# Kernel tuning notes

Measured on AMD Instinct MI355X. Metric: run time of the kernel, lower is better.

## Reference

```python
import jax, jax.numpy as jnp
import numpy as np

B, S, E, H, L, A, OBS = 4, 1024, 512, 8, 4, 8, 128
D_HEAD = E // H
EPS = 1e-6
DECAY_SCALING = 1.0


def rmsnorm(x, scale):
    return x * jax.lax.rsqrt(jnp.mean(x * x, -1, keepdims=True) + EPS) * scale


def swiglu_ffn(x, w_gate, w_lin, w_out):
    return (jax.nn.silu(x @ w_gate) * (x @ w_lin)) @ w_out


def retention(x, h, logk, w_q, w_k, w_v, w_g, w_o, gns, gnb, ts, seg):
    # x:[B,S,E]  h:[B,H,d,d]  ts/seg:[B,S] int  logk:[H]
    q = (x @ w_q).reshape(B, S, H, D_HEAD).transpose(0, 2, 1, 3)
    k = (x @ w_k).reshape(B, S, H, D_HEAD).transpose(0, 2, 1, 3) / jnp.sqrt(jnp.asarray(D_HEAD, x.dtype))
    v = (x @ w_v).reshape(B, S, H, D_HEAD).transpose(0, 2, 1, 3)
    dt = (ts[:, :, None] - ts[:, None, :]).astype(x.dtype)            # [B,S,S]
    mask = (dt >= 0) & (seg[:, :, None] == seg[:, None, :])           # timestep-causal, same episode
    dt = jnp.where(mask, dt, 0.0)
    Dm = jnp.where(mask[:, None], jnp.exp(dt[:, None] * logk[None, :, None, None]), 0.0)  # [B,H,S,S]
    scores = jnp.einsum('bhnd,bhmd->bhnm', q, k) * Dm
    inner = jnp.einsum('bhnm,bhme->bhne', scores, v)
    tsf = ts.astype(x.dtype)
    fresh = (seg == 0).astype(x.dtype)                                # prev-chunk state only valid pre-done
    xi = jnp.exp((tsf + 1.0)[:, None, :] * logk[None, :, None]) * fresh[:, None, :]  # [B,H,S]
    cross = jnp.einsum('bhn,bhnd,bhde->bhne', xi, q, h)
    ret = inner + cross                                               # [B,H,S,d]
    # chunk-final recurrent state
    tmax = tsf[:, -1]
    eta = jnp.exp((tmax[:, None] - tsf)[:, None, :] * logk[None, :, None])
    eta = eta * (seg == seg[:, -1:]).astype(x.dtype)[:, None, :]
    keep = (seg[:, -1] == 0).astype(x.dtype)
    h_decay = jnp.exp((tmax + 1.0)[:, None] * logk[None, :]) * keep[:, None]  # [B,H]
    h_new = h * h_decay[..., None, None] + jnp.einsum('bhm,bhmd,bhme->bhde', eta, k, v)
    # per-head group norm (num_groups = n_head)
    y = ret.transpose(0, 2, 1, 3)                                     # [B,S,H,d]
    mu = jnp.mean(y, -1, keepdims=True)
    var = jnp.mean((y - mu) ** 2, -1, keepdims=True)
    y = ((y - mu) * jax.lax.rsqrt(var + EPS)).reshape(B, S, E) * gns + gnb
    out = (jax.nn.silu(x @ w_g) * y) @ w_o
    return out, h_new


def forward(obs, hstate, dones, timestep_id, ln_enc_scale, w_enc, ln_shared,
            wq, wk, wv, wg, wo, gn_scale, gn_bias, ln1_s, ln2_s,
            sw_gate, sw_lin, sw_out, head_w1, head_b1, head_ln, head_w2, head_b2):
    kappas = (1.0 - jnp.exp(jnp.linspace(jnp.log(1.0 / 32.0), jnp.log(1.0 / 512.0), H))) * DECAY_SCALING
    logk = jnp.log(kappas).astype(obs.dtype)
    seg = jnp.cumsum(dones, axis=-1)
    x = jax.nn.gelu(rmsnorm(obs, ln_enc_scale) @ w_enc)               # obs encoder
    new_h = jnp.zeros_like(hstate)
    for i in range(L):
        xin = rmsnorm(x, ln_shared)
        ret, hn = retention(xin, hstate[:, :, i], logk, wq[i], wk[i], wv[i], wg[i], wo[i],
                            gn_scale[i], gn_bias[i], timestep_id, seg)
        x1 = rmsnorm(xin + ret, ln1_s[i])
        x = rmsnorm(x1 + swiglu_ffn(x1, sw_gate[i], sw_lin[i], sw_out[i]), ln2_s[i])
        new_h = new_h.at[:, :, i].set(hn)
    z = jax.nn.gelu(x @ head_w1 + head_b1)
    v_loc = rmsnorm(z, head_ln) @ head_w2 + head_b2
    return v_loc, x, new_h


def setup_inputs() -> dict:
    key = jax.random.key(0)
    ks = jax.random.split(key, 16)
    sc = 0.02
    f = jnp.float32
    return {
        'obs': jax.random.normal(ks[0], (B, S, OBS), f),
        'hstate': jax.random.normal(ks[1], (B, H, L, D_HEAD, D_HEAD), f) * 0.1,
        'dones': (jax.random.uniform(ks[2], (B, S)) < 0.01).astype(jnp.int32),
        'timestep_id': jnp.broadcast_to(jnp.repeat(jnp.arange(S // A, dtype=jnp.int32), A)[None], (B, S)),
        'ln_enc_scale': jnp.ones((OBS,), f),
        'w_enc': jax.random.normal(ks[3], (OBS, E), f) * sc,
        'ln_shared': jnp.ones((E,), f),
        'wq': jax.random.normal(ks[4], (L, E, E), f) * sc,
        'wk': jax.random.normal(ks[5], (L, E, E), f) * sc,
        'wv': jax.random.normal(ks[6], (L, E, E), f) * sc,
        'wg': jax.random.normal(ks[7], (L, E, E), f) * sc,
        'wo': jax.random.normal(ks[8], (L, E, E), f) * sc,
        'gn_scale': jnp.ones((L, E), f),
        'gn_bias': jnp.zeros((L, E), f),
        'ln1_s': jnp.ones((L, E), f),
        'ln2_s': jnp.ones((L, E), f),
        'sw_gate': jax.random.normal(ks[9], (L, E, E), f) * sc,
        'sw_lin': jax.random.normal(ks[10], (L, E, E), f) * sc,
        'sw_out': jax.random.normal(ks[11], (L, E, E), f) * sc,
        'head_w1': jax.random.normal(ks[12], (E, E), f) * sc,
        'head_b1': jnp.zeros((E,), f),
        'head_ln': jnp.ones((E,), f),
        'head_w2': jax.random.normal(ks[13], (E, 1), f) * 0.01,
        'head_b2': jnp.zeros((1,), f),
    }


def reference(obs, hstate, dones, timestep_id, ln_enc_scale, w_enc, ln_shared,
              wq, wk, wv, wg, wo, gn_scale, gn_bias, ln1_s, ln2_s,
              sw_gate, sw_lin, sw_out, head_w1, head_b1, head_ln, head_w2, head_b2):
    return forward(obs, hstate, dones, timestep_id, ln_enc_scale, w_enc, ln_shared,
                   wq, wk, wv, wg, wo, gn_scale, gn_bias, ln1_s, ln2_s,
                   sw_gate, sw_lin, sw_out, head_w1, head_b1, head_ln, head_w2, head_b2)
```

## Files before the change

kernel.cpp:

```cpp
#include <hip/hip_runtime.h>
#include <math.h>

#define BN 4
#define SN 1024
#define EN 512
#define HN 8
#define LN 4
#define DN 64
#define OBSN 128
#define NR (BN*SN)
#define NB (NR*EN)
#define EPSF 1e-6f

typedef __attribute__((ext_vector_type(8))) short short8v;
typedef __attribute__((ext_vector_type(4))) float f32x4;
typedef unsigned short u16;

__device__ __forceinline__ float logk_of(int h){
    const float start = -3.4657359027997265f;
    const float step  = -0.3960841031771117f;
    return logf(1.0f - expf(start + step*(float)h));
}
__device__ __forceinline__ float geluf(float x){
    float x3 = x*x*x;
    return 0.5f*x*(1.0f + tanhf(0.7978845608028654f*(x + 0.044715f*x3)));
}
__device__ __forceinline__ float siluf(float x){
    return x / (1.0f + expf(-x));
}
__device__ __forceinline__ u16 f2bf(float x){
    union { float f; unsigned u; } v; v.f = x;
    unsigned r = v.u + 0x7FFFu + ((v.u >> 16) & 1u);
    return (u16)(r >> 16);
}
__device__ __forceinline__ float bf2f(u16 x){
    union { unsigned u; float f; } v; v.u = ((unsigned)x)<<16;
    return v.f;
}
__device__ __forceinline__ void load_lds16(const void* g, void* l){
    __builtin_amdgcn_global_load_lds((const __attribute__((address_space(1))) void*)g,
                                     (__attribute__((address_space(3))) void*)l, 16, 0, 0);
}
__device__ __forceinline__ int swz(int r, int bo){ return r*128 + (bo ^ ((r&7)<<4)); }

__global__ void seg_kernel(const int* __restrict__ dones, int* __restrict__ seg){
    __shared__ int sm[SN];
    int b = blockIdx.x, t = threadIdx.x;
    sm[t] = dones[b*SN + t];
    __syncthreads();
    for (int off=1; off<SN; off<<=1){
        int v = (t>=off) ? sm[t-off] : 0;
        __syncthreads();
        sm[t] += v;
        __syncthreads();
    }
    seg[b*SN + t] = sm[t];
}

__global__ void wconv8_kernel(const float* w0, const float* w1, const float* w2,
                              const float* w3, const float* w4, const float* w5,
                              const float* w6, const float* w7,
                              u16* __restrict__ dst){
    __shared__ u16 tile[32][33];
    int z = blockIdx.z;
    int type = z>>2, layer = z&3;
    const float* srcs[8] = {w0,w1,w2,w3,w4,w5,w6,w7};
    const float* s = srcs[type] + (size_t)layer*EN*EN;
    u16* d = dst + ((size_t)type*LN + layer)*EN*EN;
    int k0 = blockIdx.y*32, m0 = blockIdx.x*32;
    int tx = threadIdx.x, ty = threadIdx.y;
    #pragma unroll
    for (int i=0;i<32;i+=8)
        tile[tx][ty+i] = f2bf(s[(size_t)(k0+ty+i)*EN + m0+tx]);
    __syncthreads();
    #pragma unroll
    for (int i=0;i<32;i+=8)
        d[(size_t)(m0+ty+i)*EN + k0+tx] = tile[ty+i][tx];
}
__global__ void wconv_kernel(const float* __restrict__ src, u16* __restrict__ dst,
                             int K, int M){
    __shared__ u16 tile[32][33];
    int k0 = blockIdx.y*32, m0 = blockIdx.x*32;
    int tx = threadIdx.x, ty = threadIdx.y;
    #pragma unroll
    for (int i=0;i<32;i+=8)
        tile[tx][ty+i] = f2bf(src[(size_t)(k0+ty+i)*M + m0+tx]);
    __syncthreads();
    #pragma unroll
    for (int i=0;i<32;i+=8)
        dst[(size_t)(m0+ty+i)*K + k0+tx] = tile[ty+i][tx];
}

template<int COLS, bool WF32, bool WBF>
__global__ void rmsnorm_kernel(const float* __restrict__ A,
                               const float* __restrict__ scale,
                               float* __restrict__ Of,
                               u16* __restrict__ Ob){
    constexpr int PER = COLS/64;
    int row  = blockIdx.x*4 + (threadIdx.x>>6);
    int lane = threadIdx.x & 63;
    const float* a = A + (size_t)row*COLS;
    float v[PER];
    float ss = 0.f;
    #pragma unroll
    for (int i=0;i<PER;i++){
        float x = a[lane + i*64];
        v[i] = x; ss += x*x;
    }
    #pragma unroll
    for (int off=32; off>0; off>>=1) ss += __shfl_xor(ss, off, 64);
    float rs = rsqrtf(ss*(1.0f/COLS) + EPSF);
    #pragma unroll
    for (int i=0;i<PER;i++){
        float o = v[i]*rs*scale[lane + i*64];
        if (WF32) Of[(size_t)row*COLS + lane + i*64] = o;
        if (WBF)  Ob[(size_t)row*COLS + lane + i*64] = f2bf(o);
    }
}

__device__ __forceinline__ void stage_tile(const u16* __restrict__ G, size_t rowBase,
                                           int K, int k0, u16* dst, int t){
    #pragma unroll
    for (int i=0;i<2;i++){
        int o = i*4096 + t*16;
        int grow = o>>7, gcolb = o&127;
        load_lds16(G + (rowBase+grow)*K + k0 + (gcolb>>1), (char*)dst + o);
    }
}
__device__ __forceinline__ void mma_tile(const u16* As, const u16* Bs, f32x4 acc[2][2],
                                         int wr, int wc, int lane){
    #pragma unroll
    for (int kk=0; kk<64; kk+=32){
        int kb = kk + (lane>>4)*8;
        short8v a[2], b[2];
        #pragma unroll
        for (int m=0;m<2;m++)
            a[m] = *(const short8v*)((const char*)As + (wr*32+m*16+(lane&15))*128 + kb*2);
        #pragma unroll
        for (int n=0;n<2;n++)
            b[n] = *(const short8v*)((const char*)Bs + (wc*32+n*16+(lane&15))*128 + kb*2);
        #pragma unroll
        for (int m=0;m<2;m++)
            #pragma unroll
            for (int n=0;n<2;n++)
                acc[m][n] = __builtin_amdgcn_mfma_f32_16x16x32_bf16(a[m], b[n], acc[m][n], 0,0,0);
    }
}
#define ZERO_ACC(acc) { _Pragma("unroll") for (int m=0;m<2;m++) _Pragma("unroll") for (int n=0;n<2;n++){ acc[m][n][0]=0.f;acc[m][n][1]=0.f;acc[m][n][2]=0.f;acc[m][n][3]=0.f; } }

__global__ __launch_bounds__(256) void gemm_qkvg(
    const u16* __restrict__ A,
    const u16* __restrict__ WQ, const u16* __restrict__ WK,
    const u16* __restrict__ WV, const u16* __restrict__ WG,
    u16* __restrict__ Qbb, u16* __restrict__ Kbb,
    u16* __restrict__ VtT, u16* __restrict__ KtT, float* __restrict__ Gb)
{
    __shared__ u16 As[2][64*64];
    __shared__ u16 Bs[2][4][64*64];
    int t = threadIdx.x;
    int row0 = blockIdx.y*64, col0 = blockIdx.x*64;
    int w = t>>6, lane = t&63;
    int wr = w>>1, wc = w&1;
    f32x4 accQ[2][2], accK[2][2], accV[2][2], accG[2][2];
    ZERO_ACC(accQ); ZERO_ACC(accK); ZERO_ACC(accV); ZERO_ACC(accG);
    const u16* Ws[4] = {WQ, WK, WV, WG};

    stage_tile(A, (size_t)row0, EN, 0, As[0], t);
    #pragma unroll
    for (int wt=0; wt<4; wt++) stage_tile(Ws[wt], (size_t)col0, EN, 0, Bs[0][wt], t);
    __syncthreads();
    for (int ti=0; ti<EN/64; ++ti){
        int cur = ti&1;
        if (ti+1 < EN/64){
            stage_tile(A, (size_t)row0, EN, (ti+1)*64, As[cur^1], t);
            #pragma unroll
            for (int wt=0; wt<4; wt++)
                stage_tile(Ws[wt], (size_t)col0, EN, (ti+1)*64, Bs[cur^1][wt], t);
        }
        mma_tile(As[cur], Bs[cur][0], accQ, wr, wc, lane);
        mma_tile(As[cur], Bs[cur][1], accK, wr, wc, lane);
        mma_tile(As[cur], Bs[cur][2], accV, wr, wc, lane);
        mma_tile(As[cur], Bs[cur][3], accG, wr, wc, lane);
        __syncthreads();
    }
    #pragma unroll
    for (int m=0;m<2;m++){
        #pragma unroll
        for (int n=0;n<2;n++){
            int col = col0 + wc*32 + n*16 + (lane&15);
            int rbase = row0 + wr*32 + m*16 + (lane>>4)*4;
            ushort4 pkV, pkK;
            #pragma unroll
            for (int j=0;j<4;j++){
                size_t idx = (size_t)(rbase+j)*EN + col;
                Qbb[idx] = f2bf(accQ[m][n][j]);
                float kx = accK[m][n][j]*0.125f;
                Kbb[idx] = f2bf(kx);
                ((u16*)&pkK)[j] = f2bf(kx);
                ((u16*)&pkV)[j] = f2bf(accV[m][n][j]);
                Gb[idx] = siluf(accG[m][n][j]);
            }
            int bb = rbase>>10;
            int s0 = rbase&1023;
            *(ushort4*)(VtT + ((size_t)bb*EN + col)*SN + s0) = pkV;
            *(ushort4*)(KtT + ((size_t)bb*EN + col)*SN + s0) = pkK;
        }
    }
}

__global__ __launch_bounds__(256) void gemm_swpair(
    const u16* __restrict__ A,
    const u16* __restrict__ WGt, const u16* __restrict__ WLt,
    u16* __restrict__ Out)
{
    __shared__ u16 As[2][64*64];
    __shared__ u16 Bg[2][64*64];
    __shared__ u16 Bl[2][64*64];
    int t = threadIdx.x;
    int row0 = blockIdx.y*64, col0 = blockIdx.x*64;
    int w = t>>6, lane = t&63;
    int wr = w>>1, wc = w&1;
    f32x4 accG[2][2], accL[2][2];
    ZERO_ACC(accG); ZERO_ACC(accL);
    stage_tile(A, (size_t)row0, EN, 0, As[0], t);
    stage_tile(WGt, (size_t)col0, EN, 0, Bg[0], t);
    stage_tile(WLt, (size_t)col0, EN, 0, Bl[0], t);
    __syncthreads();
    for (int ti=0; ti<EN/64; ++ti){
        int cur = ti&1;
        if (ti+1 < EN/64){
            stage_tile(A, (size_t)row0, EN, (ti+1)*64, As[cur^1], t);
            stage_tile(WGt, (size_t)col0, EN, (ti+1)*64, Bg[cur^1], t);
            stage_tile(WLt, (size_t)col0, EN, (ti+1)*64, Bl[cur^1], t);
        }
        mma_tile(As[cur], Bg[cur], accG, wr, wc, lane);
        mma_tile(As[cur], Bl[cur], accL, wr, wc, lane);
        __syncthreads();
    }
    #pragma unroll
    for (int m=0;m<2;m++){
        #pragma unroll
        for (int n=0;n<2;n++){
            int col = col0 + wc*32 + n*16 + (lane&15);
            int rbase = row0 + wr*32 + m*16 + (lane>>4)*4;
            #pragma unroll
            for (int j=0;j<4;j++){
                float x = siluf(accG[m][n][j]) * accL[m][n][j];
                Out[(size_t)(rbase+j)*EN + col] = f2bf(x);
            }
        }
    }
}

template<int ACT, bool BIASF, bool RESF, int OUTM>
__global__ __launch_bounds__(256) void gemm_bf16(
    const u16* __restrict__ A, const u16* __restrict__ Wt,
    const float* __restrict__ bias, const float* __restrict__ res,
    float* __restrict__ C, u16* __restrict__ Ob, int K, float scale)
{
    __shared__ u16 As[2][64*64];
    __shared__ u16 Bs[2][64*64];
    int t = threadIdx.x;
    int row0 = blockIdx.y*64, col0 = blockIdx.x*64;
    int w = t>>6, lane = t&63;
    int wr = w>>1, wc = w&1;
    f32x4 acc[2][2];
    ZERO_ACC(acc);
    int nt = K/64;
    stage_tile(A, (size_t)row0, K, 0, As[0], t);
    stage_tile(Wt, (size_t)col0, K, 0, Bs[0], t);
    __syncthreads();
    for (int ti=0; ti<nt; ++ti){
        int cur = ti&1;
        if (ti+1 < nt){
            stage_tile(A, (size_t)row0, K, (ti+1)*64, As[cur^1], t);
            stage_tile(Wt, (size_t)col0, K, (ti+1)*64, Bs[cur^1], t);
        }
        mma_tile(As[cur], Bs[cur], acc, wr, wc, lane);
        __syncthreads();
    }
    #pragma unroll
    for (int m=0;m<2;m++){
        #pragma unroll
        for (int n=0;n<2;n++){
            int col = col0 + wc*32 + n*16 + (lane&15);
            int rbase = row0 + wr*32 + m*16 + (lane>>4)*4;
            #pragma unroll
            for (int j=0;j<4;j++){
                float x = acc[m][n][j]*scale;
                if (BIASF) x += bias[col];
                if (ACT==1) x = siluf(x);
                if (ACT==2) x = geluf(x);
                if (RESF) x += res[(size_t)(rbase+j)*512 + col];
                if (OUTM&1) C[(size_t)(rbase+j)*512 + col] = x;
                if (OUTM&2) Ob[(size_t)(rbase+j)*512 + col] = f2bf(x);
            }
        }
    }
}

__global__ __launch_bounds__(256) void retention_mfma(
    const u16* __restrict__ Qbb, const u16* __restrict__ Kbb,
    const u16* __restrict__ VtT, const u16* __restrict__ KtT,
    const float* __restrict__ hstate, const int* __restrict__ tsid, const int* __restrict__ seg,
    const float* __restrict__ gns, const float* __restrict__ gnb,
    const float* __restrict__ Gb, u16* __restrict__ Out,
    float* __restrict__ Hout, int layer)
{
    int bh = blockIdx.y; int b = bh>>3; int h = bh&7;
    int t = threadIdx.x, lane = t&63, w = t>>6;
    __shared__ u16 Qs[64*64];
    __shared__ u16 Ks[64*64];
    __shared__ u16 Vts[64*64];
    __shared__ u16 Ps[64*64];
    __shared__ float tsq_s[64], eq_s[64], xi_s[64];
    __shared__ int   segq_s[64];
    __shared__ float tsm_s[64], em_s[64];
    __shared__ int   segm_s[64];
    float lk = logk_of(h);

    if (blockIdx.x == 0){
        float tmax = (float)tsid[b*SN + SN-1];
        int segl = seg[b*SN + SN-1];
        float* eta = (float*)Qs;
        #pragma unroll
        for (int i=0;i<4;i++){
            int m = t + i*256;
            float tsm = (float)tsid[b*SN+m];
            eta[m] = (seg[b*SN+m]==segl) ? expf((tmax - tsm)*lk) : 0.f;
        }
        f32x4 eacc[4];
        #pragma unroll
        for (int en=0;en<4;en++){ eacc[en][0]=0.f; eacc[en][1]=0.f; eacc[en][2]=0.f; eacc[en][3]=0.f; }
        for (int mt=0; mt<16; ++mt){
            int m0 = mt*64;
            __syncthreads();
            #pragma unroll
            for (int i=0;i<2;i++){
                int c = t + i*256; int r = c>>3, cb = (c&7)*16;
                int mb = m0 + (cb>>1);
                size_t g = ((size_t)(b*EN) + h*DN + r)*SN + mb;
                short8v kt = *(const short8v*)(KtT + g);
                short8v vt = *(const short8v*)(VtT + g);
                short8v ks;
                #pragma unroll
                for (int j=0;j<8;j++) ks[j] = (short)f2bf(bf2f((u16)kt[j]) * eta[mb+j]);
                *(short8v*)((char*)Ks  + swz(r,cb)) = ks;
                *(short8v*)((char*)Vts + swz(r,cb)) = vt;
            }
            __syncthreads();
            short8v a0 = *(short8v*)((char*)Ks + swz(w*16+(lane&15), (lane>>4)*16));
            short8v a1 = *(short8v*)((char*)Ks + swz(w*16+(lane&15), 64+(lane>>4)*16));
            __builtin_amdgcn_s_setprio(1);
            #pragma unroll
            for (int en=0;en<4;en++){
                short8v b0 = *(short8v*)((char*)Vts + swz(en*16+(lane&15), (lane>>4)*16));
                short8v b1 = *(short8v*)((char*)Vts + swz(en*16+(lane&15), 64+(lane>>4)*16));
                eacc[en] = __builtin_amdgcn_mfma_f32_16x16x32_bf16(a0, b0, eacc[en], 0,0,0);
                eacc[en] = __builtin_amdgcn_mfma_f32_16x16x32_bf16(a1, b1, eacc[en], 0,0,0);
            }
            __builtin_amdgcn_s_setprio(0);
        }
        float hd = (segl==0) ? expf((tmax+1.0f)*lk) : 0.f;
        const float* h0 = hstate + ((size_t)bh*LN + layer)*4096;
        float* ho = Hout + ((size_t)bh*LN + layer)*4096;
        #pragma unroll
        for (int en=0;en<4;en++){
            int e = en*16 + (lane&15);
            #pragma unroll
            for (int j=0;j<4;j++){
                int d = w*16 + (lane>>4)*4 + j;
                ho[d*64 + e] = h0[d*64 + e]*hd + eacc[en][j];
            }
        }
        return;
    }

    int tile = 16 - (int)blockIdx.x;
    int n0 = tile*64;

    #pragma unroll
    for (int i=0;i<2;i++){
        int c = t + i*256; int r = c>>3, cb = (c&7)*16;
        short8v qv = *(const short8v*)(Qbb + (size_t)(b*SN + n0 + r)*EN + h*DN + (cb>>1));
        *(short8v*)((char*)Qs + swz(r,cb)) = qv;
    }
    const float* h0 = hstate + ((size_t)bh*LN + layer)*4096;
    #pragma unroll
    for (int i=0;i<4;i++){
        int idx = t + i*256; int d = idx>>4, e0 = (idx&15)*4;
        float4 hv = *(const float4*)(h0 + d*64 + e0);
        *(u16*)((char*)Ps + swz(e0+0, 2*d)) = f2bf(hv.x);
        *(u16*)((char*)Ps + swz(e0+1, 2*d)) = f2bf(hv.y);
        *(u16*)((char*)Ps + swz(e0+2, 2*d)) = f2bf(hv.z);
        *(u16*)((char*)Ps + swz(e0+3, 2*d)) = f2bf(hv.w);
    }
    if (t<64){
        float tq = (float)tsid[b*SN+n0+t];
        int sg = seg[b*SN+n0+t];
        tsq_s[t]=tq; segq_s[t]=sg;
        eq_s[t]=expf(tq*lk);
        xi_s[t]=(sg==0)?expf((tq+1.f)*lk):0.f;
    }
    short8v kr0, kr1, vr0, vr1;
    {
        int c0 = t, c1 = t+256;
        int r0=c0>>3, cb0=(c0&7)*16, r1=c1>>3, cb1=(c1&7)*16;
        kr0 = *(const short8v*)(Kbb + (size_t)(b*SN+r0)*EN + h*DN + (cb0>>1));
        kr1 = *(const short8v*)(Kbb + (size_t)(b*SN+r1)*EN + h*DN + (cb1>>1));
        vr0 = *(const short8v*)(VtT + ((size_t)(b*EN)+h*DN+r0)*SN + (cb0>>1));
        vr1 = *(const short8v*)(VtT + ((size_t)(b*EN)+h*DN+r1)*SN + (cb1>>1));
    }
    __syncthreads();

    int qlj = w*16 + ((lane>>4)<<2);
    float tsq_r[4], eq_r[4], xi_r[4]; int sgq_r[4];
    #pragma unroll
    for (int j=0;j<4;j++){
        tsq_r[j]=tsq_s[qlj+j]; eq_r[j]=eq_s[qlj+j];
        xi_r[j]=xi_s[qlj+j];  sgq_r[j]=segq_s[qlj+j];
    }
    short8v aq0 = *(short8v*)((char*)Qs + swz(w*16+(lane&15), (lane>>4)*16));
    short8v aq1 = *(short8v*)((char*)Qs + swz(w*16+(lane&15), 64 + (lane>>4)*16));

    f32x4 oacc[4];
    {
        f32x4 cacc[4];
        #pragma unroll
        for (int en=0;en<4;en++){ cacc[en][0]=0.f; cacc[en][1]=0.f; cacc[en][2]=0.f; cacc[en][3]=0.f; }
        #pragma unroll
        for (int en=0;en<4;en++){
            short8v b0 = *(short8v*)((char*)Ps + swz(en*16+(lane&15), (lane>>4)*16));
            short8v b1 = *(short8v*)((char*)Ps + swz(en*16+(lane&15), 64+(lane>>4)*16));
            cacc[en] = __builtin_amdgcn_mfma_f32_16x16x32_bf16(aq0, b0, cacc[en], 0,0,0);
            cacc[en] = __builtin_amdgcn_mfma_f32_16x16x32_bf16(aq1, b1, cacc[en], 0,0,0);
        }
        #pragma unroll
        for (int en=0;en<4;en++)
            #pragma unroll
            for (int j=0;j<4;j++) oacc[en][j] = cacc[en][j]*xi_r[j];
    }

    for (int mt=0; mt<=tile; ++mt){
        int m0 = mt*64;
        __syncthreads();
        {
            int c0 = t, c1 = t+256;
            int r0=c0>>3, cb0=(c0&7)*16, r1=c1>>3, cb1=(c1&7)*16;
            *(short8v*)((char*)Ks  + swz(r0,cb0)) = kr0;
            *(short8v*)((char*)Ks  + swz(r1,cb1)) = kr1;
            *(short8v*)((char*)Vts + swz(r0,cb0)) = vr0;
            *(short8v*)((char*)Vts + swz(r1,cb1)) = vr1;
        }
        if (t<64){
            float tm = (float)tsid[b*SN+m0+t];
            tsm_s[t]=tm; segm_s[t]=seg[b*SN+m0+t]; em_s[t]=expf(-tm*lk);
        }
        if (mt < tile){
            int m1 = m0 + 64;
            int c0 = t, c1 = t+256;
            int r0=c0>>3, cb0=(c0&7)*16, r1=c1>>3, cb1=(c1&7)*16;
            kr0 = *(const short8v*)(Kbb + (size_t)(b*SN+m1+r0)*EN + h*DN + (cb0>>1));
            kr1 = *(const short8v*)(Kbb + (size_t)(b*SN+m1+r1)*EN + h*DN + (cb1>>1));
            vr0 = *(const short8v*)(VtT + ((size_t)(b*EN)+h*DN+r0)*SN + m1 + (cb0>>1));
            vr1 = *(const short8v*)(VtT + ((size_t)(b*EN)+h*DN+r1)*SN + m1 + (cb1>>1));
        }
        __syncthreads();
        f32x4 sacc[4];
        #pragma unroll
        for (int mn=0;mn<4;mn++){ sacc[mn][0]=0.f; sacc[mn][1]=0.f; sacc[mn][2]=0.f; sacc[mn][3]=0.f; }
        __builtin_amdgcn_s_setprio(1);
        #pragma unroll
        for (int mn=0;mn<4;mn++){
            short8v b0 = *(short8v*)((char*)Ks + swz(mn*16+(lane&15), (lane>>4)*16));
            short8v b1 = *(short8v*)((char*)Ks + swz(mn*16+(lane&15), 64+(lane>>4)*16));
            sacc[mn] = __builtin_amdgcn_mfma_f32_16x16x32_bf16(aq0, b0, sacc[mn], 0,0,0);
            sacc[mn] = __builtin_amdgcn_mfma_f32_16x16x32_bf16(aq1, b1, sacc[mn], 0,0,0);
        }
        __builtin_amdgcn_s_setprio(0);
        #pragma unroll
        for (int mn=0;mn<4;mn++){
            int m = mn*16 + (lane&15);
            float tm = tsm_s[m]; float em = em_s[m]; int sgm = segm_s[m];
            #pragma unroll
            for (int j=0;j<4;j++){
                float p = (tsq_r[j]>=tm && sgq_r[j]==sgm) ? sacc[mn][j]*eq_r[j]*em : 0.f;
                *(u16*)((char*)Ps + swz(qlj+j, 2*m)) = f2bf(p);
            }
        }
        short8v ap0 = *(short8v*)((char*)Ps + swz(w*16+(lane&15), (lane>>4)*16));
        short8v ap1 = *(short8v*)((char*)Ps + swz(w*16+(lane&15), 64+(lane>>4)*16));
        __builtin_amdgcn_s_setprio(1);
        #pragma unroll
        for (int dn=0;dn<4;dn++){
            short8v b0 = *(short8v*)((char*)Vts + swz(dn*16+(lane&15), (lane>>4)*16));
            short8v b1 = *(short8v*)((char*)Vts + swz(dn*16+(lane&15), 64+(lane>>4)*16));
            oacc[dn] = __builtin_amdgcn_mfma_f32_16x16x32_bf16(ap0, b0, oacc[dn], 0,0,0);
            oacc[dn] = __builtin_amdgcn_mfma_f32_16x16x32_bf16(ap1, b1, oacc[dn], 0,0,0);
        }
        __builtin_amdgcn_s_setprio(0);
    }

    float mu[4], rs[4];
    #pragma unroll
    for (int j=0;j<4;j++){
        float s = oacc[0][j]+oacc[1][j]+oacc[2][j]+oacc[3][j];
        #pragma unroll
        for (int off=1; off<16; off<<=1) s += __shfl_xor(s, off, 64);
        mu[j] = s*(1.0f/64.0f);
        float d0=oacc[0][j]-mu[j], d1=oacc[1][j]-mu[j], d2=oacc[2][j]-mu[j], d3=oacc[3][j]-mu[j];
        float q2 = d0*d0+d1*d1+d2*d2+d3*d3;
        #pragma unroll
        for (int off=1; off<16; off<<=1) q2 += __shfl_xor(q2, off, 64);
        rs[j] = rsqrtf(q2*(1.0f/64.0f) + EPSF);
    }
    #pragma unroll
    for (int dn=0;dn<4;dn++){
        int e = h*DN + dn*16 + (lane&15);
        float gs = gns[e], gb = gnb[e];
        #pragma unroll
        for (int j=0;j<4;j++){
            size_t row = (size_t)(b*SN + n0 + qlj + j);
            float y = (oacc[dn][j]-mu[j])*rs[j]*gs + gb;
            Out[row*EN + e] = f2bf(y * Gb[row*EN + e]);
        }
    }
}

__global__ void vloc_kernel(const float* __restrict__ ZN, const float* __restrict__ w2,
                            const float* __restrict__ b2, float* __restrict__ out){
    int row  = blockIdx.x*4 + (threadIdx.x>>6);
    int lane = threadIdx.x & 63;
    const float* z = ZN + (size_t)row*EN;
    float s = 0.f;
    #pragma unroll
    for (int i=0;i<8;i++) s += z[lane + i*64]*w2[lane + i*64];
    #pragma unroll
    for (int off=32; off>0; off>>=1) s += __shfl_xor(s, off, 64);
    if (lane==0) out[row] = s + b2[0];
}

static inline void launch_gemm(const u16* A, const u16* Wt, const float* bias,
                               const float* res, float* C, u16* Ob,
                               int K, float scale, int act, int outm, hipStream_t s){
    dim3 g(8, 64), b(256,1,1);
    if (bias)                    gemm_bf16<2,true ,false,1><<<g,b,0,s>>>(A,Wt,bias,res,C,Ob,K,scale);
    else if (res && outm==3)     gemm_bf16<0,false,true ,3><<<g,b,0,s>>>(A,Wt,bias,res,C,Ob,K,scale);
    else if (res)                gemm_bf16<0,false,true ,1><<<g,b,0,s>>>(A,Wt,bias,res,C,Ob,K,scale);
    else if (act==2)             gemm_bf16<2,false,false,1><<<g,b,0,s>>>(A,Wt,bias,res,C,Ob,K,scale);
    else                         gemm_bf16<0,false,false,1><<<g,b,0,s>>>(A,Wt,bias,res,C,Ob,K,scale);
}

extern "C" void kernel_launch(void* const* d_in, const int* in_sizes, int n_in,
                              void* d_out, int out_size, void* d_ws, size_t ws_size,
                              hipStream_t stream){
    const float* obs       = (const float*)d_in[0];
    const float* hstate    = (const float*)d_in[1];
    const int*   dones     = (const int*)  d_in[2];
    const int*   tsid      = (const int*)  d_in[3];
    const float* ln_enc    = (const float*)d_in[4];
    const float* w_enc     = (const float*)d_in[5];
    const float* ln_shared = (const float*)d_in[6];
    const float* wq        = (const float*)d_in[7];
    const float* wk        = (const float*)d_in[8];
    const float* wv        = (const float*)d_in[9];
    const float* wg        = (const float*)d_in[10];
    const float* wo        = (const float*)d_in[11];
    const float* gns       = (const float*)d_in[12];
    const float* gnb       = (const float*)d_in[13];
    const float* ln1       = (const float*)d_in[14];
    const float* ln2       = (const float*)d_in[15];
    const float* swg       = (const float*)d_in[16];
    const float* swl       = (const float*)d_in[17];
    const float* swo       = (const float*)d_in[18];
    const float* hw1       = (const float*)d_in[19];
    const float* hb1       = (const float*)d_in[20];
    const float* hln       = (const float*)d_in[21];
    const float* hw2       = (const float*)d_in[22];
    const float* hb2       = (const float*)d_in[23];

    float* out_v = (float*)d_out;
    float* out_x = out_v + NR;
    float* out_h = out_x + (size_t)NR*EN;

    float* ws    = (float*)d_ws;
    float* XIN   = ws + 0*(size_t)NB;
    float* Qb    = ws + 1*(size_t)NB;
    float* Kb    = ws + 2*(size_t)NB;
    float* Vb    = ws + 3*(size_t)NB;
    float* Gb    = ws + 4*(size_t)NB;
    float* Yb    = ws + 5*(size_t)NB;
    int*   seg   = (int*)(ws + 6*(size_t)NB);
    u16* wtb  = (u16*)(seg + NR);
    const size_t WEm = (size_t)EN*EN;
    u16* wqT   = wtb;
    u16* wkT   = wqT + 4*WEm;
    u16* wvT   = wkT + 4*WEm;
    u16* wgT   = wvT + 4*WEm;
    u16* woT   = wgT + 4*WEm;
    u16* sgT   = woT + 4*WEm;
    u16* slT   = sgT + 4*WEm;
    u16* soT   = slT + 4*WEm;
    u16* wencT = soT + 4*WEm;
    u16* w1T   = wencT + (size_t)EN*OBSN;
    u16* S1b   = w1T + WEm;
    u16* S2b   = S1b + (size_t)NB;
    u16* encb  = S2b + (size_t)NB;
    u16* Qbb   = encb + (size_t)NR*OBSN;
    u16* Kbb   = Qbb + (size_t)NB;
    u16* VtT   = (u16*)Qb;
    u16* KtT   = VtT + (size_t)NB;

    seg_kernel<<<BN, SN, 0, stream>>>(dones, seg);

    {
        dim3 tb(32,8,1);
        wconv8_kernel<<<dim3(16,16,32), tb, 0, stream>>>(wq,wk,wv,wg,wo,swg,swl,swo, wtb);
        wconv_kernel<<<dim3(16,4,1),  tb, 0, stream>>>(w_enc, wencT, OBSN, EN);
        wconv_kernel<<<dim3(16,16,1), tb, 0, stream>>>(hw1,   w1T,   EN, EN);
    }

    rmsnorm_kernel<OBSN,false,true><<<NR/4, 256, 0, stream>>>(obs, ln_enc, nullptr, encb);
    launch_gemm(encb, wencT, nullptr, nullptr, out_x, nullptr, OBSN, 1.f, 2, 1, stream);

    for (int l=0; l<LN; ++l){
        rmsnorm_kernel<EN,true,true><<<NR/4, 256, 0, stream>>>(out_x, ln_shared, XIN, S1b);
        gemm_qkvg<<<dim3(8,64), 256, 0, stream>>>(S1b,
            wqT + l*WEm, wkT + l*WEm, wvT + l*WEm, wgT + l*WEm,
            Qbb, Kbb, VtT, KtT, Gb);
        retention_mfma<<<dim3(17, BN*HN), 256, 0, stream>>>(
            Qbb, Kbb, VtT, KtT, hstate, tsid, seg, gns + l*EN, gnb + l*EN,
            Gb, S2b, out_h, l);
        launch_gemm(S2b, woT + l*WEm, nullptr, XIN, Qb, nullptr, EN, 1.f, 0, 1, stream);
        rmsnorm_kernel<EN,true,true><<<NR/4, 256, 0, stream>>>(Qb, ln1 + l*EN, Kb, S1b);
        gemm_swpair<<<dim3(8,64), 256, 0, stream>>>(S1b, sgT + l*WEm, slT + l*WEm, S2b);
        launch_gemm(S2b, soT + l*WEm, nullptr, Kb, Qb, nullptr, EN, 1.f, 0, 1, stream);
        if (l == LN-1)
            rmsnorm_kernel<EN,true,true ><<<NR/4, 256, 0, stream>>>(Qb, ln2 + l*EN, out_x, S1b);
        else
            rmsnorm_kernel<EN,true,false><<<NR/4, 256, 0, stream>>>(Qb, ln2 + l*EN, out_x, nullptr);
    }

    launch_gemm(S1b, w1T, hb1, nullptr, Yb, nullptr, EN, 1.f, 2, 1, stream);
    rmsnorm_kernel<EN,true,false><<<NR/4, 256, 0, stream>>>(Yb, hln, XIN, nullptr);
    vloc_kernel<<<NR/4, 256, 0, stream>>>(XIN, hw2, hb2, out_v);
}
```

Measured before the change: 436.4 us.

## Fold RMSNorm scales into weights and fuse norms into GEMM epilogues

Removes the standalone RMSNorm kernels inside the layer loop. Per-column norm scales (ln_shared·ln2 and ln1) are folded into the bf16 weights during conversion. Per-row inverse RMS factors come from sum-of-squares that the producing GEMM epilogues accumulate with atomics, and the consuming GEMMs apply them. This avoids several full fp32 read/write passes per layer, at the cost of atomic traffic, an extra memset, and rounding differences from scaling weights before bf16 conversion.

```diff
diff --git a/kernel.cpp b/kernel.cpp
--- a/kernel.cpp
+++ b/kernel.cpp
@@ -43,6 +43,12 @@
 }
 __device__ __forceinline__ int swz(int r, int bo){ return r*128 + (bo ^ ((r&7)<<4)); }
 
+__device__ __forceinline__ float rx_of(int mode, const float* ssA, const float* ssB, int row){
+    float rn = rsqrtf(ssA[row]*(1.f/512.f) + EPSF);
+    if (mode==0) return rn;
+    return rn*rsqrtf(rn*rn*ssB[row]*(1.f/512.f) + EPSF);
+}
+
 __global__ void seg_kernel(const int* __restrict__ dones, int* __restrict__ seg){
     __shared__ int sm[SN];
     int b = blockIdx.x, t = threadIdx.x;
@@ -57,9 +63,18 @@
     seg[b*SN + t] = sm[t];
 }
 
+__global__ void lnvq_kernel(const float* __restrict__ lnsh, const float* __restrict__ ln2,
+                            float* __restrict__ lnvq){
+    int k = threadIdx.x;
+    #pragma unroll
+    for (int l=0;l<LN;l++)
+        lnvq[l*EN + k] = lnsh[k] * (l ? ln2[(l-1)*EN + k] : 1.f);
+}
+
 __global__ void wconv8_kernel(const float* w0, const float* w1, const float* w2,
                               const float* w3, const float* w4, const float* w5,
                               const float* w6, const float* w7,
+                              const float* __restrict__ lnvq, const float* __restrict__ ln1,
                               u16* __restrict__ dst){
     __shared__ u16 tile[32][33];
     int z = blockIdx.z;
@@ -70,8 +85,13 @@
     int k0 = blockIdx.y*32, m0 = blockIdx.x*32;
     int tx = threadIdx.x, ty = threadIdx.y;
     #pragma unroll
-    for (int i=0;i<32;i+=8)
-        tile[tx][ty+i] = f2bf(s[(size_t)(k0+ty+i)*EN + m0+tx]);
+    for (int i=0;i<32;i+=8){
+        int k = k0+ty+i;
+        float sc = 1.f;
+        if (type<4) sc = lnvq[layer*EN + k];
+        else if (type==5 || type==6) sc = ln1[layer*EN + k];
+        tile[tx][ty+i] = f2bf(s[(size_t)k*EN + m0+tx]*sc);
+    }
     __syncthreads();
     #pragma unroll
     for (int i=0;i<32;i+=8)
@@ -91,31 +111,18 @@
         dst[(size_t)(m0+ty+i)*K + k0+tx] = tile[ty+i][tx];
 }
 
-template<int COLS, bool WF32, bool WBF>
-__global__ void rmsnorm_kernel(const float* __restrict__ A,
-                               const float* __restrict__ scale,
-                               float* __restrict__ Of,
-                               u16* __restrict__ Ob){
-    constexpr int PER = COLS/64;
+__global__ void rmsobs_kernel(const float* __restrict__ A, const float* __restrict__ scale,
+                              u16* __restrict__ Ob){
     int row  = blockIdx.x*4 + (threadIdx.x>>6);
     int lane = threadIdx.x & 63;
-    const float* a = A + (size_t)row*COLS;
-    float v[PER];
-    float ss = 0.f;
-    #pragma unroll
-    for (int i=0;i<PER;i++){
-        float x = a[lane + i*64];
-        v[i] = x; ss += x*x;
-    }
+    const float* a = A + (size_t)row*OBSN;
+    float v0 = a[lane], v1 = a[lane+64];
+    float ss = v0*v0 + v1*v1;
     #pragma unroll
     for (int off=32; off>0; off>>=1) ss += __shfl_xor(ss, off, 64);
-    float rs = rsqrtf(ss*(1.0f/COLS) + EPSF);
-    #pragma unroll
-    for (int i=0;i<PER;i++){
-        float o = v[i]*rs*scale[lane + i*64];
-        if (WF32) Of[(size_t)row*COLS + lane + i*64] = o;
-        if (WBF)  Ob[(size_t)row*COLS + lane + i*64] = f2bf(o);
-    }
+    float rs = rsqrtf(ss*(1.0f/OBSN) + EPSF);
+    Ob[(size_t)row*OBSN + lane]      = f2bf(v0*rs*scale[lane]);
+    Ob[(size_t)row*OBSN + lane + 64] = f2bf(v1*rs*scale[lane+64]);
 }
 
 __device__ __forceinline__ void stage_tile(const u16* __restrict__ G, size_t rowBase,
@@ -148,10 +155,60 @@
 }
 #define ZERO_ACC(acc) { _Pragma("unroll") for (int m=0;m<2;m++) _Pragma("unroll") for (int n=0;n<2;n++){ acc[m][n][0]=0.f;acc[m][n][1]=0.f;acc[m][n][2]=0.f;acc[m][n][3]=0.f; } }
 
+__device__ __forceinline__ void ss_atomic(float v, float* __restrict__ ss, int row, int lane){
+    #pragma unroll
+    for (int off=1; off<16; off<<=1) v += __shfl_xor(v, off, 16);
+    if ((lane&15)==0) atomicAdd(&ss[row], v);
+}
+
+__global__ __launch_bounds__(256) void gemm_enc(
+    const u16* __restrict__ A, const u16* __restrict__ Wt,
+    float* __restrict__ Xf, u16* __restrict__ Xb, float* __restrict__ ssA)
+{
+    __shared__ u16 As[2][64*64];
+    __shared__ u16 Bs[2][64*64];
+    int t = threadIdx.x;
+    int row0 = blockIdx.y*64, col0 = blockIdx.x*64;
+    int w = t>>6, lane = t&63;
+    int wr = w>>1, wc = w&1;
+    f32x4 acc[2][2];
+    ZERO_ACC(acc);
+    stage_tile(A, (size_t)row0, OBSN, 0, As[0], t);
+    stage_tile(Wt, (size_t)col0, OBSN, 0, Bs[0], t);
+    __syncthreads();
+    for (int ti=0; ti<OBSN/64; ++ti){
+        int cur = ti&1;
+        if (ti+1 < OBSN/64){
+            stage_tile(A, (size_t)row0, OBSN, (ti+1)*64, As[cur^1], t);
+            stage_tile(Wt, (size_t)col0, OBSN, (ti+1)*64, Bs[cur^1], t);
+        }
+        mma_tile(As[cur], Bs[cur], acc, wr, wc, lane);
+        __syncthreads();
+    }
+    #pragma unroll
+    for (int m=0;m<2;m++){
+        #pragma unroll
+        for (int j=0;j<4;j++){
+            int row = row0 + wr*32 + m*16 + (lane>>4)*4 + j;
+            float sv = 0.f;
+            #pragma unroll
+            for (int n=0;n<2;n++){
+                int col = col0 + wc*32 + n*16 + (lane&15);
+                float x = geluf(acc[m][n][j]);
+                Xf[(size_t)row*EN + col] = x;
+                Xb[(size_t)row*EN + col] = f2bf(x);
+                sv += x*x;
+            }
+            ss_atomic(sv, ssA, row, lane);
+        }
+    }
+}
+
 __global__ __launch_bounds__(256) void gemm_qkvg(
     const u16* __restrict__ A,
     const u16* __restrict__ WQ, const u16* __restrict__ WK,
     const u16* __restrict__ WV, const u16* __restrict__ WG,
+    const float* __restrict__ ssA, const float* __restrict__ ssB, int mode,
     u16* __restrict__ Qbb, u16* __restrict__ Kbb,
     u16* __restrict__ VtT, u16* __restrict__ KtT, float* __restrict__ Gb)
 {
@@ -183,6 +240,12 @@
         mma_tile(As[cur], Bs[cur][3], accG, wr, wc, lane);
         __syncthreads();
     }
+    float rxv[2][4];
+    #pragma unroll
+    for (int m=0;m<2;m++)
+        #pragma unroll
+        for (int j=0;j<4;j++)
+            rxv[m][j] = rx_of(mode, ssA, ssB, row0 + wr*32 + m*16 + (lane>>4)*4 + j);
     #pragma unroll
     for (int m=0;m<2;m++){
         #pragma unroll
@@ -192,13 +255,14 @@
             ushort4 pkV, pkK;
             #pragma unroll
             for (int j=0;j<4;j++){
+                float rx = rxv[m][j];
                 size_t idx = (size_t)(rbase+j)*EN + col;
-                Qbb[idx] = f2bf(accQ[m][n][j]);
-                float kx = accK[m][n][j]*0.125f;
+                Qbb[idx] = f2bf(rx*accQ[m][n][j]);
+                float kx = rx*accK[m][n][j]*0.125f;
                 Kbb[idx] = f2bf(kx);
                 ((u16*)&pkK)[j] = f2bf(kx);
-                ((u16*)&pkV)[j] = f2bf(accV[m][n][j]);
-                Gb[idx] = siluf(accG[m][n][j]);
+                ((u16*)&pkV)[j] = f2bf(rx*accV[m][n][j]);
+                Gb[idx] = siluf(rx*accG[m][n][j]);
             }
             int bb = rbase>>10;
             int s0 = rbase&1023;
@@ -208,10 +272,57 @@
     }
 }
 
+__global__ __launch_bounds__(256) void gemm_wo(
+    const u16* __restrict__ A, const u16* __restrict__ Wt,
+    const float* __restrict__ Xf, const float* __restrict__ lnv,
+    const float* __restrict__ ssA, const float* __restrict__ ssB, int mode,
+    float* __restrict__ Y1f, u16* __restrict__ Y1b, float* __restrict__ ss1)
+{
+    __shared__ u16 As[2][64*64];
+    __shared__ u16 Bs[2][64*64];
+    int t = threadIdx.x;
+    int row0 = blockIdx.y*64, col0 = blockIdx.x*64;
+    int w = t>>6, lane = t&63;
+    int wr = w>>1, wc = w&1;
+    f32x4 acc[2][2];
+    ZERO_ACC(acc);
+    stage_tile(A, (size_t)row0, EN, 0, As[0], t);
+    stage_tile(Wt, (size_t)col0, EN, 0, Bs[0], t);
+    __syncthreads();
+    for (int ti=0; ti<EN/64; ++ti){
+        int cur = ti&1;
+        if (ti+1 < EN/64){
+            stage_tile(A, (size_t)row0, EN, (ti+1)*64, As[cur^1], t);
+            stage_tile(Wt, (size_t)col0, EN, (ti+1)*64, Bs[cur^1], t);
+        }
+        mma_tile(As[cur], Bs[cur], acc, wr, wc, lane);
+        __syncthreads();
+    }
+    #pragma unroll
+    for (int m=0;m<2;m++){
+        #pragma unroll
+        for (int j=0;j<4;j++){
+            int row = row0 + wr*32 + m*16 + (lane>>4)*4 + j;
+            float rx = rx_of(mode, ssA, ssB, row);
+            float sv = 0.f;
+            #pragma unroll
+            for (int n=0;n<2;n++){
+                int col = col0 + wc*32 + n*16 + (lane&15);
+                size_t idx = (size_t)row*EN + col;
+                float x = acc[m][n][j] + rx*lnv[col]*Xf[idx];
+                Y1f[idx] = x;
+                Y1b[idx] = f2bf(x);
+                sv += x*x;
+            }
+            ss_atomic(sv, ss1, row, lane);
+        }
+    }
+}
+
 __global__ __launch_bounds__(256) void gemm_swpair(
     const u16* __restrict__ A,
     const u16* __restrict__ WGt, const u16* __restrict__ WLt,
-    u16* __restrict__ Out)
+    const float* __restrict__ ss1, u16* __restrict__ Out)
 {
     __shared__ u16 As[2][64*64];
     __shared__ u16 Bg[2][64*64];
@@ -245,18 +356,20 @@
             int rbase = row0 + wr*32 + m*16 + (lane>>4)*4;
             #pragma unroll
             for (int j=0;j<4;j++){
-                float x = siluf(accG[m][n][j]) * accL[m][n][j];
+                float r1 = rx_of(0, ss1, nullptr, rbase+j);
+                float x = siluf(r1*accG[m][n][j]) * (r1*accL[m][n][j]);
                 Out[(size_t)(rbase+j)*EN + col] = f2bf(x);
             }
         }
     }
 }
 
-template<int ACT, bool BIASF, bool RESF, int OUTM>
-__global__ __launch_bounds__(256) void gemm_bf16(
+__global__ __launch_bounds__(256) void gemm_swo(
     const u16* __restrict__ A, const u16* __restrict__ Wt,
-    const float* __restrict__ bias, const float* __restrict__ res,
-    float* __restrict__ C, u16* __restrict__ Ob, int K, float scale)
+    const float* __restrict__ Y1f, const float* __restrict__ ln1,
+    const float* __restrict__ ss1, const float* __restrict__ ln2,
+    float* __restrict__ Xf, u16* __restrict__ Xb,
+    float* __restrict__ ssA, float* __restrict__ ssB)
 {
     __shared__ u16 As[2][64*64];
     __shared__ u16 Bs[2][64*64];
@@ -266,15 +379,62 @@
     int wr = w>>1, wc = w&1;
     f32x4 acc[2][2];
     ZERO_ACC(acc);
-    int nt = K/64;
-    stage_tile(A, (size_t)row0, K, 0, As[0], t);
-    stage_tile(Wt, (size_t)col0, K, 0, Bs[0], t);
-    __syncthreads();
-    for (int ti=0; ti<nt; ++ti){
+    stage_tile(A, (size_t)row0, EN, 0, As[0], t);
+    stage_tile(Wt, (size_t)col0, EN, 0, Bs[0], t);
+    __syncthreads();
+    for (int ti=0; ti<EN/64; ++ti){
         int cur = ti&1;
-        if (ti+1 < nt){
-            stage_tile(A, (size_t)row0, K, (ti+1)*64, As[cur^1], t);
-            stage_tile(Wt, (size_t)col0, K, (ti+1)*64, Bs[cur^1], t);
+        if (ti+1 < EN/64){
+            stage_tile(A, (size_t)row0, EN, (ti+1)*64, As[cur^1], t);
+            stage_tile(Wt, (size_t)col0, EN, (ti+1)*64, Bs[cur^1], t);
+        }
+        mma_tile(As[cur], Bs[cur], acc, wr, wc, lane);
+        __syncthreads();
+    }
+    #pragma unroll
+    for (int m=0;m<2;m++){
+        #pragma unroll
+        for (int j=0;j<4;j++){
+            int row = row0 + wr*32 + m*16 + (lane>>4)*4 + j;
+            float r1 = rx_of(0, ss1, nullptr, row);
+            float svA = 0.f, svB = 0.f;
+            #pragma unroll
+            for (int n=0;n<2;n++){
+                int col = col0 + wc*32 + n*16 + (lane&15);
+                size_t idx = (size_t)row*EN + col;
+                float x = acc[m][n][j] + r1*ln1[col]*Y1f[idx];
+                Xf[idx] = x;
+                Xb[idx] = f2bf(x);
+                svA += x*x;
+                float xw = x*ln2[col];
+                svB += xw*xw;
+            }
+            ss_atomic(svA, ssA, row, lane);
+            ss_atomic(svB, ssB, row, lane);
+        }
+    }
+}
+
+__global__ __launch_bounds__(256) void gemm_head(
+    const u16* __restrict__ A, const u16* __restrict__ Wt,
+    const float* __restrict__ bias, float* __restrict__ C)
+{
+    __shared__ u16 As[2][64*64];
+    __shared__ u16 Bs[2][64*64];
+    int t = threadIdx.x;
+    int row0 = blockIdx.y*64, col0 = blockIdx.x*64;
+    int w = t>>6, lane = t&63;
+    int wr = w>>1, wc = w&1;
+    f32x4 acc[2][2];
+    ZERO_ACC(acc);
+    stage_tile(A, (size_t)row0, EN, 0, As[0], t);
+    stage_tile(Wt, (size_t)col0, EN, 0, Bs[0], t);
+    __syncthreads();
+    for (int ti=0; ti<EN/64; ++ti){
+        int cur = ti&1;
+        if (ti+1 < EN/64){
+            stage_tile(A, (size_t)row0, EN, (ti+1)*64, As[cur^1], t);
+            stage_tile(Wt, (size_t)col0, EN, (ti+1)*64, Bs[cur^1], t);
         }
         mma_tile(As[cur], Bs[cur], acc, wr, wc, lane);
         __syncthreads();
@@ -286,15 +446,8 @@
             int col = col0 + wc*32 + n*16 + (lane&15);
             int rbase = row0 + wr*32 + m*16 + (lane>>4)*4;
             #pragma unroll
-            for (int j=0;j<4;j++){
-                float x = acc[m][n][j]*scale;
-                if (BIASF) x += bias[col];
-                if (ACT==1) x = siluf(x);
-                if (ACT==2) x = geluf(x);
-                if (RESF) x += res[(size_t)(rbase+j)*512 + col];
-                if (OUTM&1) C[(size_t)(rbase+j)*512 + col] = x;
-                if (OUTM&2) Ob[(size_t)(rbase+j)*512 + col] = f2bf(x);
-            }
+            for (int j=0;j<4;j++)
+                C[(size_t)(rbase+j)*EN + col] = geluf(acc[m][n][j] + bias[col]);
         }
     }
 }
@@ -527,28 +680,41 @@
     }
 }
 
-__global__ void vloc_kernel(const float* __restrict__ ZN, const float* __restrict__ w2,
-                            const float* __restrict__ b2, float* __restrict__ out){
+__global__ void xout_kernel(const float* __restrict__ Xf, const float* __restrict__ ssA,
+                            const float* __restrict__ ln23,
+                            float* __restrict__ out_x, u16* __restrict__ Xb){
     int row  = blockIdx.x*4 + (threadIdx.x>>6);
     int lane = threadIdx.x & 63;
-    const float* z = ZN + (size_t)row*EN;
-    float s = 0.f;
-    #pragma unroll
-    for (int i=0;i<8;i++) s += z[lane + i*64]*w2[lane + i*64];
-    #pragma unroll
-    for (int off=32; off>0; off>>=1) s += __shfl_xor(s, off, 64);
-    if (lane==0) out[row] = s + b2[0];
-}
-
-static inline void launch_gemm(const u16* A, const u16* Wt, const float* bias,
-                               const float* res, float* C, u16* Ob,
-                               int K, float scale, int act, int outm, hipStream_t s){
-    dim3 g(8, 64), b(256,1,1);
-    if (bias)                    gemm_bf16<2,true ,false,1><<<g,b,0,s>>>(A,Wt,bias,res,C,Ob,K,scale);
-    else if (res && outm==3)     gemm_bf16<0,false,true ,3><<<g,b,0,s>>>(A,Wt,bias,res,C,Ob,K,scale);
-    else if (res)                gemm_bf16<0,false,true ,1><<<g,b,0,s>>>(A,Wt,bias,res,C,Ob,K,scale);
-    else if (act==2)             gemm_bf16<2,false,false,1><<<g,b,0,s>>>(A,Wt,bias,res,C,Ob,K,scale);
-    else                         gemm_bf16<0,false,false,1><<<g,b,0,s>>>(A,Wt,bias,res,C,Ob,K,scale);
+    float rn = rsqrtf(ssA[row]*(1.f/512.f) + EPSF);
+    #pragma unroll
+    for (int i=0;i<8;i++){
+        int col = lane + i*64;
+        float x = rn * Xf[(size_t)row*EN + col] * ln23[col];
+        out_x[(size_t)row*EN + col] = x;
+        Xb[(size_t)row*EN + col] = f2bf(x);
+    }
+}
+
+__global__ void vloc_kernel(const float* __restrict__ Z, const float* __restrict__ hln,
+                            const float* __restrict__ w2, const float* __restrict__ b2,
+                            float* __restrict__ out){
+    int row  = blockIdx.x*4 + (threadIdx.x>>6);
+    int lane = threadIdx.x & 63;
+    const float* z = Z + (size_t)row*EN;
+    float ss = 0.f, dot = 0.f;
+    #pragma unroll
+    for (int i=0;i<8;i++){
+        int col = lane + i*64;
+        float zv = z[col];
+        ss += zv*zv;
+        dot += zv*hln[col]*w2[col];
+    }
+    #pragma unroll
+    for (int off=32; off>0; off>>=1){
+        ss += __shfl_xor(ss, off, 64);
+        dot += __shfl_xor(dot, off, 64);
+    }
+    if (lane==0) out[row] = rsqrtf(ss*(1.f/512.f)+EPSF)*dot + b2[0];
 }
 
 extern "C" void kernel_launch(void* const* d_in, const int* in_sizes, int n_in,
@@ -584,64 +750,67 @@
     float* out_h = out_x + (size_t)NR*EN;
 
     float* ws    = (float*)d_ws;
-    float* XIN   = ws + 0*(size_t)NB;
-    float* Qb    = ws + 1*(size_t)NB;
-    float* Kb    = ws + 2*(size_t)NB;
-    float* Vb    = ws + 3*(size_t)NB;
-    float* Gb    = ws + 4*(size_t)NB;
-    float* Yb    = ws + 5*(size_t)NB;
-    int*   seg   = (int*)(ws + 6*(size_t)NB);
+    float* Xf    = ws + 0*(size_t)NB;
+    float* Qs32  = ws + 1*(size_t)NB;
+    float* Y1f   = ws + 2*(size_t)NB;
+    float* Gb    = ws + 3*(size_t)NB;
+    float* Zb    = ws + 4*(size_t)NB;
+    int*   seg   = (int*)(ws + 5*(size_t)NB);
     u16* wtb  = (u16*)(seg + NR);
     const size_t WEm = (size_t)EN*EN;
     u16* wqT   = wtb;
-    u16* wkT   = wqT + 4*WEm;
-    u16* wvT   = wkT + 4*WEm;
-    u16* wgT   = wvT + 4*WEm;
-    u16* woT   = wgT + 4*WEm;
-    u16* sgT   = woT + 4*WEm;
-    u16* slT   = sgT + 4*WEm;
-    u16* soT   = slT + 4*WEm;
-    u16* wencT = soT + 4*WEm;
+    u16* woT   = wtb + 4*4*WEm;
+    u16* wencT = wtb + 8*4*WEm;
     u16* w1T   = wencT + (size_t)EN*OBSN;
-    u16* S1b   = w1T + WEm;
-    u16* S2b   = S1b + (size_t)NB;
-    u16* encb  = S2b + (size_t)NB;
+    u16* Xb    = w1T + WEm;
+    u16* S2b   = Xb  + (size_t)NB;
+    u16* Y1b   = S2b + (size_t)NB;
+    u16* encb  = Y1b + (size_t)NB;
     u16* Qbb   = encb + (size_t)NR*OBSN;
     u16* Kbb   = Qbb + (size_t)NB;
-    u16* VtT   = (u16*)Qb;
+    u16* VtT   = (u16*)Qs32;
     u16* KtT   = VtT + (size_t)NB;
+    float* ssBase = (float*)(Kbb + (size_t)NB);
+    float* ssA   = ssBase;
+    float* ssB   = ssA + 5*NR;
+    float* ss1   = ssB + 5*NR;
+    float* lnvq  = ss1 + 4*NR;
+
+    hipMemsetAsync(ssBase, 0, (5*NR + 5*NR + 4*NR)*sizeof(float), stream);
 
     seg_kernel<<<BN, SN, 0, stream>>>(dones, seg);
-
+    lnvq_kernel<<<1, EN, 0, stream>>>(ln_shared, ln2, lnvq);
     {
         dim3 tb(32,8,1);
-        wconv8_kernel<<<dim3(16,16,32), tb, 0, stream>>>(wq,wk,wv,wg,wo,swg,swl,swo, wtb);
+        wconv8_kernel<<<dim3(16,16,32), tb, 0, stream>>>(wq,wk,wv,wg,wo,swg,swl,swo, lnvq, ln1, wtb);
         wconv_kernel<<<dim3(16,4,1),  tb, 0, stream>>>(w_enc, wencT, OBSN, EN);
         wconv_kernel<<<dim3(16,16,1), tb, 0, stream>>>(hw1,   w1T,   EN, EN);
     }
 
-    rmsnorm_kernel<OBSN,false,true><<<NR/4, 256, 0, stream>>>(obs, ln_enc, nullptr, encb);
-    launch_gemm(encb, wencT, nullptr, nullptr, out_x, nullptr, OBSN, 1.f, 2, 1, stream);
+    rmsobs_kernel<<<NR/4, 256, 0, stream>>>(obs, ln_enc, encb);
+    gemm_enc<<<dim3(8,64), 256, 0, stream>>>(encb, wencT, Xf, Xb, ssA);
 
     for (int l=0; l<LN; ++l){
-        rmsnorm_kernel<EN,true,true><<<NR/4, 256, 0, stream>>>(out_x, ln_shared, XIN, S1b);
-        gemm_qkvg<<<dim3(8,64), 256, 0, stream>>>(S1b,
-            wqT + l*WEm, wkT + l*WEm, wvT + l*WEm, wgT + l*WEm,
-            Qbb, Kbb, VtT, KtT, Gb);
+        int mode = (l==0) ? 0 : 1;
+        const float* sA = ssA + l*NR;
+        const float* sB = ssB + l*NR;
+        float* s1 = ss1 + l*NR;
+        gemm_qkvg<<<dim3(8,64), 256, 0, stream>>>(Xb,
+            wtb + (0*LN+l)*WEm, wtb + (1*LN+l)*WEm, wtb + (2*LN+l)*WEm, wtb + (3*LN+l)*WEm,
+            sA, sB, mode, Qbb, Kbb, VtT, KtT, Gb);
         retention_mfma<<<dim3(17, BN*HN), 256, 0, stream>>>(
             Qbb, Kbb, VtT, KtT, hstate, tsid, seg, gns + l*EN, gnb + l*EN,
             Gb, S2b, out_h, l);
-        launch_gemm(S2b, woT + l*WEm, nullptr, XIN, Qb, nullptr, EN, 1.f, 0, 1, stream);
-        rmsnorm_kernel<EN,true,true><<<NR/4, 256, 0, stream>>>(Qb, ln1 + l*EN, Kb, S1b);
-        gemm_swpair<<<dim3(8,64), 256, 0, stream>>>(S1b, sgT + l*WEm, slT + l*WEm, S2b);
-        launch_gemm(S2b, soT + l*WEm, nullptr, Kb, Qb, nullptr, EN, 1.f, 0, 1, stream);
-        if (l == LN-1)
-            rmsnorm_kernel<EN,true,true ><<<NR/4, 256, 0, stream>>>(Qb, ln2 + l*EN, out_x, S1b);
-        else
-            rmsnorm_kernel<EN,true,false><<<NR/4, 256, 0, stream>>>(Qb, ln2 + l*EN, out_x, nullptr);
-    }
-
-    launch_gemm(S1b, w1T, hb1, nullptr, Yb, nullptr, EN, 1.f, 2, 1, stream);
-    rmsnorm_kernel<EN,true,false><<<NR/4, 256, 0, stream>>>(Yb, hln, XIN, nullptr);
-    vloc_kernel<<<NR/4, 256, 0, stream>>>(XIN, hw2, hb2, out_v);
-}
+        gemm_wo<<<dim3(8,64), 256, 0, stream>>>(S2b, wtb + (4*LN+l)*WEm,
+            Xf, lnvq + l*EN, sA, sB, mode, Y1f, Y1b, s1);
+        gemm_swpair<<<dim3(8,64), 256, 0, stream>>>(Y1b,
+            wtb + (5*LN+l)*WEm, wtb + (6*LN+l)*WEm, s1, S2b);
+        gemm_swo<<<dim3(8,64), 256, 0, stream>>>(S2b, wtb + (7*LN+l)*WEm,
+            Y1f, ln1 + l*EN, s1, ln2 + l*EN,
+            Xf, Xb, ssA + (l+1)*NR, ssB + (l+1)*NR);
+    }
+
+    xout_kernel<<<NR/4, 256, 0, stream>>>(Xf, ssA + LN*NR, ln2 + 3*EN, out_x, Xb);
+    gemm_head<<<dim3(8,64), 256, 0, stream>>>(Xb, w1T, hb1, Zb);
+    vloc_kernel<<<NR/4, 256, 0, stream>>>(Zb, hln, hw2, hb2, out_v);
+}
```

After: 458.4 us. 5.0% more time.
